# Optimization experiments

Hardware: AMD Instinct MI355X
Metric: run time of the kernel (lower is better)

## Reference

```python
import jax, jax.numpy as jnp
import numpy as np

B, CIN, COUT, RES, WDIM, K, GN_GROUPS = 8, 512, 512, 64, 512, 3, 32


def setup_inputs() -> dict:
    key = jax.random.key(0)
    ks = jax.random.split(key, 6)
    return dict(
        x=jax.random.normal(ks[0], (B, CIN, RES, RES), jnp.float32),
        w=jax.random.normal(ks[1], (B, WDIM), jnp.float32),
        noise=jax.random.normal(ks[2], (B, 1, RES, RES), jnp.float32),
        weight=jax.random.normal(ks[3], (COUT, CIN, K, K), jnp.float32),
        bias=jnp.zeros((COUT,), jnp.float32),
        affine_W=jax.random.normal(ks[4], (3 * CIN, WDIM), jnp.float32),
        affine_b=jnp.ones((3 * CIN,), jnp.float32),  # bias_init=1
        gn_weight=jnp.ones((CIN,), jnp.float32),
        gn_bias=jnp.zeros((CIN,), jnp.float32),
        gamma=jnp.full((1, COUT, 1, 1), 1e-5, jnp.float32),  # layer_scale_init
        noise_strength=jnp.asarray(0.1, jnp.float32),
    )


def _group_norm_f32(x, weight, bias, groups=GN_GROUPS, eps=1e-5):
    # GroupNorm_float32: normalize in float32, cast back to x.dtype
    b, c, h, w = x.shape
    xf = x.astype(jnp.float32).reshape(b, groups, c // groups, h, w)
    mu = xf.mean(axis=(2, 3, 4), keepdims=True)
    var = xf.var(axis=(2, 3, 4), keepdims=True)
    xn = ((xf - mu) * jax.lax.rsqrt(var + eps)).reshape(b, c, h, w)
    return (xn * weight[None, :, None, None] + bias[None, :, None, None]).astype(x.dtype)


def reference(x, w, noise, weight, bias, affine_W, affine_b, gn_weight, gn_bias, gamma, noise_strength):
    b, cin, h, wd = x.shape
    cout, _, kh, kw = weight.shape
    # StyleSplit: FullyConnectedLayer (weight scaled by 1/sqrt(in_features)) then m1*m2+m3
    s = w @ (affine_W.T / jnp.sqrt(jnp.float32(w.shape[1]))) + affine_b  # [B, 3*Cin]
    m1, m2, m3 = jnp.split(s, 3, axis=1)
    styles = m1 * m2 + m3  # [B, Cin]
    # residual path: GroupNorm (float32) first
    xn = _group_norm_f32(x, gn_weight, gn_bias)
    # modulated_conv2d (fused path): per-sample modulate + demodulate
    wmod = weight[None] * styles[:, None, :, None, None]                 # [B,Cout,Cin,K,K]
    dcoef = jax.lax.rsqrt(jnp.sum(jnp.square(wmod), axis=(2, 3, 4)) + 1e-8)  # [B,Cout]
    wmod = wmod * dcoef[:, :, None, None, None]
    # grouped conv with groups = batch (StyleGAN batch-as-groups trick)
    xg = xn.reshape(1, b * cin, h, wd)
    wg = wmod.reshape(b * cout, cin, kh, kw)
    pad = kh // 2
    y = jax.lax.conv_general_dilated(
        xg, wg, window_strides=(1, 1), padding=[(pad, pad), (pad, pad)],
        dimension_numbers=('NCHW', 'OIHW', 'NCHW'), feature_group_count=b)
    y = y.reshape(b, cout, h, wd)
    # noise injection
    y = y + noise * noise_strength
    # fused bias + lrelu with gain = bias_def_gain['lrelu'] * gain = sqrt(2) * 2
    act_gain = np.sqrt(2.0) * 2.0
    y = jax.nn.leaky_relu(y + bias[None, :, None, None], 0.2) * act_gain
    # layer-scale + residual (residual uses the normalized x) * sqrt(2)
    y = (gamma * y + xn) * np.sqrt(2.0)
    return y
```

## Files before the change

kernel.cpp:

```cpp
#include <hip/hip_runtime.h>
#include <hip/hip_bf16.h>

typedef short short8 __attribute__((ext_vector_type(8)));
typedef float f32x4 __attribute__((ext_vector_type(4)));

#define SWZ(c) (((c) & 3) ^ (((c) >> 2) & 3))

static __device__ __forceinline__ unsigned short f2bf(float f) {
    union { float f; unsigned u; } v; v.f = f;
    unsigned r = v.u + 0x7FFFu + ((v.u >> 16) & 1u);
    return (unsigned short)(r >> 16);
}

static __device__ __forceinline__ void gload16(const void* g, void* l) {
    __builtin_amdgcn_global_load_lds(
        (const __attribute__((address_space(1))) unsigned int*)g,
        (__attribute__((address_space(3))) unsigned int*)l, 16, 0, 0);
}

__global__ __launch_bounds__(256) void stylesk(
    const float* __restrict__ w, const float* __restrict__ affW,
    const float* __restrict__ affb, float* __restrict__ styles)
{
    int bx = blockIdx.x, b = blockIdx.y;
    int lane = threadIdx.x & 63, wv = threadIdx.x >> 6;
    float wr[8];
    const float* wb = w + b * 512 + lane * 8;
#pragma unroll
    for (int r = 0; r < 8; ++r) wr[r] = wb[r];
    for (int ii = 0; ii < 4; ++ii) {
        int i = bx * 16 + wv * 4 + ii;
        float d[3];
#pragma unroll
        for (int jj = 0; jj < 3; ++jj) {
            const float* a = affW + (size_t)(jj * 512 + i) * 512 + lane * 8;
            float dd = 0.f;
#pragma unroll
            for (int r = 0; r < 8; ++r) dd += wr[r] * a[r];
            for (int off = 32; off; off >>= 1) dd += __shfl_xor(dd, off);
            d[jj] = dd;
        }
        if (lane == 0) {
            const float inv = 0.044194173824159216f;
            float s0 = d[0] * inv + affb[i];
            float s1 = d[1] * inv + affb[512 + i];
            float s2 = d[2] * inv + affb[1024 + i];
            styles[b * 512 + i] = s0 * s1 + s2;
        }
    }
}

__global__ __launch_bounds__(256) void gnstats(
    const float* __restrict__ x, float* __restrict__ meanv, float* __restrict__ rstdv)
{
    int bx = blockIdx.x, t = threadIdx.x;
    const float4* p = (const float4*)(x + (size_t)bx * 65536);
    float s = 0.f, q = 0.f;
#pragma unroll 4
    for (int k = 0; k < 64; ++k) {
        float4 v = p[t + (k << 8)];
        s += v.x + v.y + v.z + v.w;
        q += v.x * v.x + v.y * v.y + v.z * v.z + v.w * v.w;
    }
    for (int off = 32; off; off >>= 1) { s += __shfl_xor(s, off); q += __shfl_xor(q, off); }
    __shared__ float rs[4], rq[4];
    if ((t & 63) == 0) { rs[t >> 6] = s; rq[t >> 6] = q; }
    __syncthreads();
    if (t == 0) {
        float S = rs[0] + rs[1] + rs[2] + rs[3];
        float Q = rq[0] + rq[1] + rq[2] + rq[3];
        float mu = S * (1.f / 65536.f);
        float var = Q * (1.f / 65536.f) - mu * mu;
        meanv[bx] = mu;
        rstdv[bx] = rsqrtf(var + 1e-5f);
    }
}

__global__ __launch_bounds__(256) void dcoefk(
    const float* __restrict__ weight, const float* __restrict__ styles,
    float* __restrict__ dcoef)
{
    __shared__ float st2[8 * 512];
    __shared__ float red[32];
    int co = blockIdx.x, t = threadIdx.x;
    for (int i = t; i < 4096; i += 256) { float s = styles[i]; st2[i] = s * s; }
    __syncthreads();
    float p[8] = {0, 0, 0, 0, 0, 0, 0, 0};
#pragma unroll
    for (int half = 0; half < 2; ++half) {
        int ci = t * 2 + half;
        const float* wp = weight + ((size_t)co * 512 + ci) * 9;
        float wsq = 0.f;
#pragma unroll
        for (int k = 0; k < 9; ++k) wsq += wp[k] * wp[k];
#pragma unroll
        for (int b = 0; b < 8; ++b) p[b] += wsq * st2[b * 512 + ci];
    }
    int lane = t & 63, wv = t >> 6;
#pragma unroll
    for (int b = 0; b < 8; ++b) {
        float v = p[b];
        for (int off = 32; off; off >>= 1) v += __shfl_xor(v, off);
        if (lane == 0) red[wv * 8 + b] = v;
    }
    __syncthreads();
    if (t < 8) {
        float s = red[t] + red[8 + t] + red[16 + t] + red[24 + t];
        dcoef[t * 512 + co] = rsqrtf(s + 1e-8f);
    }
}

__global__ __launch_bounds__(256) void packk(
    const float* __restrict__ weight, unsigned short* __restrict__ wpk)
{
    __shared__ float ld[9 * 128];
    int co = blockIdx.x, c4 = blockIdx.y, t = threadIdx.x;
    const float* src = weight + (size_t)co * 4608 + c4 * 1152;
    for (int f = t; f < 1152; f += 256)
        ld[(f % 9) * 128 + (f / 9)] = src[f];
    __syncthreads();
    unsigned short* dst = wpk + (size_t)co * 4608 + c4 * 128;
    for (int f = t; f < 1152; f += 256) {
        int tap = f >> 7, ci = f & 127;
        dst[tap * 512 + ci] = f2bf(ld[tap * 128 + ci]);
    }
}

__global__ __launch_bounds__(256) void modpack(
    const float* __restrict__ x, const float* __restrict__ styles,
    const float* __restrict__ gnw, const float* __restrict__ gnb,
    const float* __restrict__ meanv, const float* __restrict__ rstdv,
    unsigned short* __restrict__ xm)
{
    __shared__ float sA[512], sB[512];
    __shared__ unsigned short tr[32 * 520];
    int t = threadIdx.x;
    int px0 = blockIdx.x * 32, b = blockIdx.y;
    for (int i = t; i < 512; i += 256) {
        int g = i >> 4;
        float mu = meanv[b * 32 + g], r = rstdv[b * 32 + g];
        float st = styles[b * 512 + i];
        float a = r * gnw[i];
        sA[i] = a * st;
        sB[i] = (gnb[i] - mu * a) * st;
    }
    __syncthreads();
    int p = t & 31, cb = t >> 5;
    const float* xb = x + (size_t)b * 512 * 4096 + px0 + p;
#pragma unroll 4
    for (int it = 0; it < 64; ++it) {
        int ci = cb + (it << 3);
        float v = xb[(size_t)ci * 4096];
        tr[p * 520 + ci] = f2bf(v * sA[ci] + sB[ci]);
    }
    __syncthreads();
    int gran = t & 63;
#pragma unroll
    for (int k = 0; k < 8; ++k) {
        int pl = k * 4 + (t >> 6);
        short8 v = *(const short8*)&tr[pl * 520 + gran * 8];
        *(short8*)&xm[((size_t)(b * 4096 + px0 + pl) << 9) + gran * 8] = v;
    }
}

__global__ __launch_bounds__(512, 2) void conv3(
    const unsigned short* __restrict__ xm, const unsigned short* __restrict__ wpk,
    const unsigned short* __restrict__ zp,
    const float* __restrict__ x, const float* __restrict__ noise,
    const float* __restrict__ bias, const float* __restrict__ gnw,
    const float* __restrict__ gnb, const float* __restrict__ gamma,
    const float* __restrict__ dcoef, const float* __restrict__ meanv,
    const float* __restrict__ rstdv, const float* __restrict__ nsp,
    float* __restrict__ out)
{
    extern __shared__ char smem[];
    char* wlds = smem;
    char* ilds = smem + 49152;

    const int tid = threadIdx.x, lane = tid & 63, wv = tid >> 6;
    const int ct = blockIdx.x, pt = blockIdx.y, b = blockIdx.z;
    const int co0 = ct * 128, h0 = pt * 8;
    const int wm = wv >> 2, wn = wv & 3;
    const int lm = lane & 15, lg = lane >> 4;

    if (tid < 160) {
        int sel = tid / 80, rem = tid % 80;
        int r = rem >> 3, col = ((rem >> 2) & 1) * 65, g = rem & 3;
        *(short8*)(ilds + sel * 42240 + r * 4224 + col * 64 + g * 16) = (short8)0;
    }

    const unsigned short* wsrc_fix[3]; int wdst_off[3];
#pragma unroll
    for (int q = 0; q < 3; ++q) {
        int k = q * 8 + wv;
        int id = k * 64 + lane;
        int dxid = id >> 9, co = (id >> 2) & 127, g = (id & 3) ^ SWZ(co);
        wsrc_fix[q] = wpk + (size_t)(co0 + co) * 4608 + dxid * 512 + g * 8;
        wdst_off[q] = k * 1024;
    }
    const unsigned short* isrc_fix[5]; int idst_off[5];
#pragma unroll
    for (int q = 0; q < 5; ++q) {
        int k = q * 8 + wv;
        int r = k >> 2, chunk = k & 3;
        int idx = chunk * 64 + lane;
        int cimg = idx >> 2, gs = (idx & 3) ^ SWZ(cimg + 1);
        int imgrow = h0 - 1 + r;
        isrc_fix[q] = ((unsigned)imgrow < 64u)
            ? xm + (((size_t)(b * 4096 + imgrow * 64 + cimg)) << 9) + gs * 8
            : zp;
        idst_off[q] = r * 4224 + 64 + chunk * 1024;
    }

    int aoff[4];
#pragma unroll
    for (int m = 0; m < 4; ++m) {
        int col = wm * 64 + m * 16 + lm;
        aoff[m] = col * 64 + (lg ^ SWZ(col)) * 16;
    }
    int boff[3][4];
#pragma unroll
    for (int dx = 0; dx < 3; ++dx)
#pragma unroll
        for (int nc = 0; nc < 4; ++nc) {
            int c = nc * 16 + lm + dx;
            boff[dx][nc] = c * 64 + (lg ^ SWZ(c)) * 16;
        }

    f32x4 acc[4][8];
#pragma unroll
    for (int m = 0; m < 4; ++m)
#pragma unroll
        for (int n = 0; n < 8; ++n) acc[m][n] = (f32x4){0.f, 0.f, 0.f, 0.f};

#pragma unroll
    for (int q = 0; q < 3; ++q) gload16(wsrc_fix[q], wlds + wdst_off[q]);
#pragma unroll
    for (int q = 0; q < 5; ++q) gload16(isrc_fix[q], ilds + idst_off[q]);
    __syncthreads();

    int cc = 0, dy = 0;
    for (int p = 0; p < 48; ++p) {
        int dyn = dy + 1, ccn = cc;
        if (dyn == 3) { dyn = 0; ccn = cc + 1; }
        if (p < 47) {
            int wadd = dyn * 1536 + ccn * 32;
            char* wd = wlds + ((p + 1) & 1) * 24576;
#pragma unroll
            for (int q = 0; q < 3; ++q) gload16(wsrc_fix[q] + wadd, wd + wdst_off[q]);
        }
        if (dy == 0 && cc < 15) {
            int iadd = (cc + 1) * 32;
            char* idp = ilds + ((cc + 1) & 1) * 42240;
#pragma unroll
            for (int q = 0; q < 5; ++q) gload16(isrc_fix[q] + iadd, idp + idst_off[q]);
        }
        char* wbase = wlds + (p & 1) * 24576;
        char* ibase = ilds + (cc & 1) * 42240 + (2 * wn + dy) * 4224;
#pragma unroll
        for (int dx = 0; dx < 3; ++dx) {
            short8 af[4], bv[8];
#pragma unroll
            for (int m = 0; m < 4; ++m)
                af[m] = *(const short8*)(wbase + dx * 8192 + aoff[m]);
#pragma unroll
            for (int n = 0; n < 8; ++n)
                bv[n] = *(const short8*)(ibase + (n >> 2) * 4224 + boff[dx][n & 3]);
#pragma unroll
            for (int m = 0; m < 4; ++m)
#pragma unroll
                for (int n = 0; n < 8; ++n)
                    acc[m][n] = __builtin_amdgcn_mfma_f32_16x16x32_bf16(
                        af[m], bv[n], acc[m][n], 0, 0, 0);
        }
        __syncthreads();
        dy = dyn; cc = ccn;
    }

    const float nsv = *nsp;
#pragma unroll
    for (int m = 0; m < 4; ++m) {
#pragma unroll
        for (int n = 0; n < 8; ++n) {
            int pix = (h0 + 2 * wn + (n >> 2)) * 64 + (n & 3) * 16 + lm;
            float nz = noise[b * 4096 + pix] * nsv;
#pragma unroll
            for (int j = 0; j < 4; ++j) {
                int co = co0 + wm * 64 + m * 16 + lg * 4 + j;
                int gidx = co >> 4;
                float v = acc[m][n][j] * dcoef[b * 512 + co] + nz + bias[co];
                float act = (v > 0.f ? v : 0.2f * v) * 2.8284271247461903f;
                float xv = x[((size_t)(b * 512 + co)) * 4096 + pix];
                float xn = (xv - meanv[b * 32 + gidx]) * rstdv[b * 32 + gidx] * gnw[co] + gnb[co];
                out[((size_t)(b * 512 + co)) * 4096 + pix] =
                    (gamma[co] * act + xn) * 1.4142135623730951f;
            }
        }
    }
}

extern "C" void kernel_launch(void* const* d_in, const int* in_sizes, int n_in,
                              void* d_out, int out_size, void* d_ws, size_t ws_size,
                              hipStream_t stream) {
    const float* x      = (const float*)d_in[0];
    const float* w      = (const float*)d_in[1];
    const float* noise  = (const float*)d_in[2];
    const float* weight = (const float*)d_in[3];
    const float* bias   = (const float*)d_in[4];
    const float* affW   = (const float*)d_in[5];
    const float* affb   = (const float*)d_in[6];
    const float* gnw    = (const float*)d_in[7];
    const float* gnb    = (const float*)d_in[8];
    const float* gamma  = (const float*)d_in[9];
    const float* nsp    = (const float*)d_in[10];
    float* out = (float*)d_out;

    char* ws = (char*)d_ws;
    float* styles = (float*)(ws + 0);
    float* dcoef  = (float*)(ws + 16384);
    float* meanv  = (float*)(ws + 32768);
    float* rstdv  = (float*)(ws + 33792);
    unsigned short* zp  = (unsigned short*)(ws + 34816);
    unsigned short* wpk = (unsigned short*)(ws + 38912);
    unsigned short* xm  = (unsigned short*)(ws + 4757504);

    hipMemsetAsync(zp, 0, 4096, stream);

    hipFuncSetAttribute(reinterpret_cast<const void*>(conv3),
                        hipFuncAttributeMaxDynamicSharedMemorySize, 135168);

    stylesk<<<dim3(32, 8), 256, 0, stream>>>(w, affW, affb, styles);
    gnstats<<<dim3(256), 256, 0, stream>>>(x, meanv, rstdv);
    packk<<<dim3(512, 4), 256, 0, stream>>>(weight, wpk);
    dcoefk<<<dim3(512), 256, 0, stream>>>(weight, styles, dcoef);
    modpack<<<dim3(128, 8), 256, 0, stream>>>(x, styles, gnw, gnb, meanv, rstdv, xm);
    conv3<<<dim3(4, 8, 8), 512, 133632, stream>>>(xm, wpk, zp, x, noise, bias, gnw, gnb,
                                                  gamma, dcoef, meanv, rstdv, nsp, out);
}
```

Measured before the change: 309.5 us.

## Merge prep kernels and triple-buffer conv weight staging with manual waitcnt pipeline

The five small preprocessing kernels and the memset become two launches that dispatch on block index: stats, styles, weight pack and zero fill in the first, dcoef and activation modpack in the second. This cuts launch gaps. The conv main loop is unrolled into explicit phases per dy, with a third weight LDS buffer and manual s_waitcnt vmcnt/s_barrier in place of __syncthreads. It also interleaves LDS fragment loads with MFMAs under s_setprio so global prefetch runs further ahead. LDS use rises to about 158KB per block, which may limit occupancy, and the hand-counted vmcnt values risk subtle races.

```diff
diff --git a/kernel.cpp b/kernel.cpp
--- a/kernel.cpp
+++ b/kernel.cpp
@@ -5,6 +5,7 @@
 typedef float f32x4 __attribute__((ext_vector_type(4)));
 
 #define SWZ(c) (((c) & 3) ^ (((c) >> 2) & 3))
+#define UNROLL _Pragma("unroll")
 
 static __device__ __forceinline__ unsigned short f2bf(float f) {
     union { float f; unsigned u; } v; v.f = f;
@@ -18,150 +19,189 @@
         (__attribute__((address_space(3))) unsigned int*)l, 16, 0, 0);
 }
 
-__global__ __launch_bounds__(256) void stylesk(
-    const float* __restrict__ w, const float* __restrict__ affW,
-    const float* __restrict__ affb, float* __restrict__ styles)
+__global__ __launch_bounds__(256) void prep1(
+    const float* __restrict__ x, const float* __restrict__ w,
+    const float* __restrict__ affW, const float* __restrict__ affb,
+    const float* __restrict__ weight,
+    float* __restrict__ styles, float* __restrict__ meanv,
+    float* __restrict__ rstdv, unsigned short* __restrict__ wpk,
+    unsigned short* __restrict__ zp)
 {
-    int bx = blockIdx.x, b = blockIdx.y;
-    int lane = threadIdx.x & 63, wv = threadIdx.x >> 6;
-    float wr[8];
-    const float* wb = w + b * 512 + lane * 8;
-#pragma unroll
-    for (int r = 0; r < 8; ++r) wr[r] = wb[r];
-    for (int ii = 0; ii < 4; ++ii) {
-        int i = bx * 16 + wv * 4 + ii;
-        float d[3];
-#pragma unroll
-        for (int jj = 0; jj < 3; ++jj) {
-            const float* a = affW + (size_t)(jj * 512 + i) * 512 + lane * 8;
-            float dd = 0.f;
-#pragma unroll
-            for (int r = 0; r < 8; ++r) dd += wr[r] * a[r];
-            for (int off = 32; off; off >>= 1) dd += __shfl_xor(dd, off);
-            d[jj] = dd;
-        }
-        if (lane == 0) {
-            const float inv = 0.044194173824159216f;
-            float s0 = d[0] * inv + affb[i];
-            float s1 = d[1] * inv + affb[512 + i];
-            float s2 = d[2] * inv + affb[1024 + i];
-            styles[b * 512 + i] = s0 * s1 + s2;
-        }
-    }
-}
-
-__global__ __launch_bounds__(256) void gnstats(
-    const float* __restrict__ x, float* __restrict__ meanv, float* __restrict__ rstdv)
-{
-    int bx = blockIdx.x, t = threadIdx.x;
-    const float4* p = (const float4*)(x + (size_t)bx * 65536);
-    float s = 0.f, q = 0.f;
+    __shared__ float ld[9 * 128];
+    __shared__ float rs[4], rq[4];
+    const int bid = blockIdx.x, t = threadIdx.x;
+
+    if (bid < 256) {
+        const float4* p = (const float4*)(x + (size_t)bid * 65536);
+        float s = 0.f, q = 0.f;
 #pragma unroll 4
-    for (int k = 0; k < 64; ++k) {
-        float4 v = p[t + (k << 8)];
-        s += v.x + v.y + v.z + v.w;
-        q += v.x * v.x + v.y * v.y + v.z * v.z + v.w * v.w;
-    }
-    for (int off = 32; off; off >>= 1) { s += __shfl_xor(s, off); q += __shfl_xor(q, off); }
-    __shared__ float rs[4], rq[4];
-    if ((t & 63) == 0) { rs[t >> 6] = s; rq[t >> 6] = q; }
-    __syncthreads();
-    if (t == 0) {
-        float S = rs[0] + rs[1] + rs[2] + rs[3];
-        float Q = rq[0] + rq[1] + rq[2] + rq[3];
-        float mu = S * (1.f / 65536.f);
-        float var = Q * (1.f / 65536.f) - mu * mu;
-        meanv[bx] = mu;
-        rstdv[bx] = rsqrtf(var + 1e-5f);
-    }
-}
-
-__global__ __launch_bounds__(256) void dcoefk(
-    const float* __restrict__ weight, const float* __restrict__ styles,
-    float* __restrict__ dcoef)
+        for (int k = 0; k < 64; ++k) {
+            float4 v = p[t + (k << 8)];
+            s += v.x + v.y + v.z + v.w;
+            q += v.x * v.x + v.y * v.y + v.z * v.z + v.w * v.w;
+        }
+        for (int off = 32; off; off >>= 1) { s += __shfl_xor(s, off); q += __shfl_xor(q, off); }
+        if ((t & 63) == 0) { rs[t >> 6] = s; rq[t >> 6] = q; }
+        __syncthreads();
+        if (t == 0) {
+            float S = rs[0] + rs[1] + rs[2] + rs[3];
+            float Q = rq[0] + rq[1] + rq[2] + rq[3];
+            float mu = S * (1.f / 65536.f);
+            float var = Q * (1.f / 65536.f) - mu * mu;
+            meanv[bid] = mu;
+            rstdv[bid] = rsqrtf(var + 1e-5f);
+        }
+    } else if (bid < 512) {
+        int idx = bid - 256, bx = idx & 31, b = idx >> 5;
+        int lane = t & 63, wv = t >> 6;
+        float wr[8];
+        const float* wb = w + b * 512 + lane * 8;
+        UNROLL for (int r = 0; r < 8; ++r) wr[r] = wb[r];
+        for (int ii = 0; ii < 4; ++ii) {
+            int i = bx * 16 + wv * 4 + ii;
+            float d[3];
+            UNROLL for (int jj = 0; jj < 3; ++jj) {
+                const float* a = affW + (size_t)(jj * 512 + i) * 512 + lane * 8;
+                float dd = 0.f;
+                UNROLL for (int r = 0; r < 8; ++r) dd += wr[r] * a[r];
+                for (int off = 32; off; off >>= 1) dd += __shfl_xor(dd, off);
+                d[jj] = dd;
+            }
+            if (lane == 0) {
+                const float inv = 0.044194173824159216f;
+                float s0 = d[0] * inv + affb[i];
+                float s1 = d[1] * inv + affb[512 + i];
+                float s2 = d[2] * inv + affb[1024 + i];
+                styles[b * 512 + i] = s0 * s1 + s2;
+            }
+        }
+    } else if (bid < 2560) {
+        int idx = bid - 512, co = idx >> 2, c4 = idx & 3;
+        const float* src = weight + (size_t)co * 4608 + c4 * 1152;
+        for (int f = t; f < 1152; f += 256)
+            ld[(f % 9) * 128 + (f / 9)] = src[f];
+        __syncthreads();
+        unsigned short* dst = wpk + (size_t)co * 4608 + c4 * 128;
+        for (int f = t; f < 1152; f += 256) {
+            int tap = f >> 7, ci = f & 127;
+            dst[tap * 512 + ci] = f2bf(ld[tap * 128 + ci]);
+        }
+    } else {
+        *(short8*)&zp[t * 8] = (short8)0;
+    }
+}
+
+__global__ __launch_bounds__(256) void prep2(
+    const float* __restrict__ x, const float* __restrict__ weight,
+    const float* __restrict__ styles, const float* __restrict__ gnw,
+    const float* __restrict__ gnb, const float* __restrict__ meanv,
+    const float* __restrict__ rstdv,
+    float* __restrict__ dcoef, unsigned short* __restrict__ xm)
 {
     __shared__ float st2[8 * 512];
     __shared__ float red[32];
-    int co = blockIdx.x, t = threadIdx.x;
-    for (int i = t; i < 4096; i += 256) { float s = styles[i]; st2[i] = s * s; }
-    __syncthreads();
-    float p[8] = {0, 0, 0, 0, 0, 0, 0, 0};
-#pragma unroll
-    for (int half = 0; half < 2; ++half) {
-        int ci = t * 2 + half;
-        const float* wp = weight + ((size_t)co * 512 + ci) * 9;
-        float wsq = 0.f;
-#pragma unroll
-        for (int k = 0; k < 9; ++k) wsq += wp[k] * wp[k];
-#pragma unroll
-        for (int b = 0; b < 8; ++b) p[b] += wsq * st2[b * 512 + ci];
-    }
-    int lane = t & 63, wv = t >> 6;
-#pragma unroll
-    for (int b = 0; b < 8; ++b) {
-        float v = p[b];
-        for (int off = 32; off; off >>= 1) v += __shfl_xor(v, off);
-        if (lane == 0) red[wv * 8 + b] = v;
-    }
-    __syncthreads();
-    if (t < 8) {
-        float s = red[t] + red[8 + t] + red[16 + t] + red[24 + t];
-        dcoef[t * 512 + co] = rsqrtf(s + 1e-8f);
-    }
-}
-
-__global__ __launch_bounds__(256) void packk(
-    const float* __restrict__ weight, unsigned short* __restrict__ wpk)
-{
-    __shared__ float ld[9 * 128];
-    int co = blockIdx.x, c4 = blockIdx.y, t = threadIdx.x;
-    const float* src = weight + (size_t)co * 4608 + c4 * 1152;
-    for (int f = t; f < 1152; f += 256)
-        ld[(f % 9) * 128 + (f / 9)] = src[f];
-    __syncthreads();
-    unsigned short* dst = wpk + (size_t)co * 4608 + c4 * 128;
-    for (int f = t; f < 1152; f += 256) {
-        int tap = f >> 7, ci = f & 127;
-        dst[tap * 512 + ci] = f2bf(ld[tap * 128 + ci]);
-    }
-}
-
-__global__ __launch_bounds__(256) void modpack(
-    const float* __restrict__ x, const float* __restrict__ styles,
-    const float* __restrict__ gnw, const float* __restrict__ gnb,
-    const float* __restrict__ meanv, const float* __restrict__ rstdv,
-    unsigned short* __restrict__ xm)
-{
     __shared__ float sA[512], sB[512];
     __shared__ unsigned short tr[32 * 520];
-    int t = threadIdx.x;
-    int px0 = blockIdx.x * 32, b = blockIdx.y;
-    for (int i = t; i < 512; i += 256) {
-        int g = i >> 4;
-        float mu = meanv[b * 32 + g], r = rstdv[b * 32 + g];
-        float st = styles[b * 512 + i];
-        float a = r * gnw[i];
-        sA[i] = a * st;
-        sB[i] = (gnb[i] - mu * a) * st;
-    }
-    __syncthreads();
-    int p = t & 31, cb = t >> 5;
-    const float* xb = x + (size_t)b * 512 * 4096 + px0 + p;
+    const int bid = blockIdx.x, t = threadIdx.x;
+
+    if (bid < 512) {
+        int co = bid;
+        for (int i = t; i < 4096; i += 256) { float s = styles[i]; st2[i] = s * s; }
+        __syncthreads();
+        float p[8] = {0, 0, 0, 0, 0, 0, 0, 0};
+        UNROLL for (int half = 0; half < 2; ++half) {
+            int ci = t * 2 + half;
+            const float* wp = weight + ((size_t)co * 512 + ci) * 9;
+            float wsq = 0.f;
+            UNROLL for (int k = 0; k < 9; ++k) wsq += wp[k] * wp[k];
+            UNROLL for (int b = 0; b < 8; ++b) p[b] += wsq * st2[b * 512 + ci];
+        }
+        int lane = t & 63, wv = t >> 6;
+        UNROLL for (int b = 0; b < 8; ++b) {
+            float v = p[b];
+            for (int off = 32; off; off >>= 1) v += __shfl_xor(v, off);
+            if (lane == 0) red[wv * 8 + b] = v;
+        }
+        __syncthreads();
+        if (t < 8) {
+            float s = red[t] + red[8 + t] + red[16 + t] + red[24 + t];
+            dcoef[t * 512 + co] = rsqrtf(s + 1e-8f);
+        }
+    } else {
+        int idx = bid - 512, b = idx >> 7, px0 = (idx & 127) * 32;
+        for (int i = t; i < 512; i += 256) {
+            int g = i >> 4;
+            float mu = meanv[b * 32 + g], r = rstdv[b * 32 + g];
+            float st = styles[b * 512 + i];
+            float a = r * gnw[i];
+            sA[i] = a * st;
+            sB[i] = (gnb[i] - mu * a) * st;
+        }
+        __syncthreads();
+        int p = t & 31, cb = t >> 5;
+        const float* xb = x + (size_t)b * 512 * 4096 + px0 + p;
 #pragma unroll 4
-    for (int it = 0; it < 64; ++it) {
-        int ci = cb + (it << 3);
-        float v = xb[(size_t)ci * 4096];
-        tr[p * 520 + ci] = f2bf(v * sA[ci] + sB[ci]);
-    }
-    __syncthreads();
-    int gran = t & 63;
-#pragma unroll
-    for (int k = 0; k < 8; ++k) {
-        int pl = k * 4 + (t >> 6);
-        short8 v = *(const short8*)&tr[pl * 520 + gran * 8];
-        *(short8*)&xm[((size_t)(b * 4096 + px0 + pl) << 9) + gran * 8] = v;
-    }
-}
+        for (int it = 0; it < 64; ++it) {
+            int ci = cb + (it << 3);
+            float v = xb[(size_t)ci * 4096];
+            tr[p * 520 + ci] = f2bf(v * sA[ci] + sB[ci]);
+        }
+        __syncthreads();
+        int gran = t & 63;
+        UNROLL for (int k = 0; k < 8; ++k) {
+            int pl = k * 4 + (t >> 6);
+            short8 v = *(const short8*)&tr[pl * 520 + gran * 8];
+            *(short8*)&xm[((size_t)(b * 4096 + px0 + pl) << 9) + gran * 8] = v;
+        }
+    }
+}
+
+#define STAGE_W(SLOT, CC_, DY_)                                                 \
+    { char* wd_ = wlds + (SLOT) * 24576; int wadd_ = (DY_) * 1536 + (CC_) * 32; \
+      UNROLL for (int q = 0; q < 3; ++q)                                        \
+          gload16(wsrc_fix[q] + wadd_, wd_ + wdst_off[q]); }
+
+#define STAGE_I(CC_)                                                            \
+    { char* id_ = ilds + ((CC_) & 1) * 42240; int iadd_ = (CC_) * 32;           \
+      UNROLL for (int q = 0; q < 5; ++q)                                        \
+          gload16(isrc_fix[q] + iadd_, id_ + idst_off[q]); }
+
+#define PHASE(DY, CCSEL, VMN, STAGES_)                                          \
+  {                                                                             \
+    char* wbase = wlds + (DY) * 24576;                                          \
+    char* ibase = ilds + (CCSEL) * 42240 + (2 * wn + (DY)) * 4224;              \
+    short8 a0[4], b0[8], a1[4], b1[8], a2[4], b2[8];                            \
+    UNROLL for (int m = 0; m < 4; ++m)                                          \
+        a0[m] = *(const short8*)(wbase + aoff[m]);                              \
+    UNROLL for (int n = 0; n < 8; ++n)                                          \
+        b0[n] = *(const short8*)(ibase + (n >> 2) * 4224 + boff[0][n & 3]);     \
+    STAGES_                                                                     \
+    asm volatile("s_barrier" ::: "memory");                                     \
+    UNROLL for (int m = 0; m < 4; ++m)                                          \
+        a1[m] = *(const short8*)(wbase + 8192 + aoff[m]);                       \
+    UNROLL for (int n = 0; n < 8; ++n)                                          \
+        b1[n] = *(const short8*)(ibase + (n >> 2) * 4224 + boff[1][n & 3]);     \
+    __builtin_amdgcn_s_setprio(1);                                              \
+    UNROLL for (int m = 0; m < 4; ++m)                                          \
+        UNROLL for (int n = 0; n < 8; ++n)                                      \
+            acc[m][n] = __builtin_amdgcn_mfma_f32_16x16x32_bf16(                \
+                a0[m], b0[n], acc[m][n], 0, 0, 0);                              \
+    UNROLL for (int m = 0; m < 4; ++m)                                          \
+        a2[m] = *(const short8*)(wbase + 16384 + aoff[m]);                      \
+    UNROLL for (int n = 0; n < 8; ++n)                                          \
+        b2[n] = *(const short8*)(ibase + (n >> 2) * 4224 + boff[2][n & 3]);     \
+    UNROLL for (int m = 0; m < 4; ++m)                                          \
+        UNROLL for (int n = 0; n < 8; ++n)                                      \
+            acc[m][n] = __builtin_amdgcn_mfma_f32_16x16x32_bf16(                \
+                a1[m], b1[n], acc[m][n], 0, 0, 0);                              \
+    UNROLL for (int m = 0; m < 4; ++m)                                          \
+        UNROLL for (int n = 0; n < 8; ++n)                                      \
+            acc[m][n] = __builtin_amdgcn_mfma_f32_16x16x32_bf16(                \
+                a2[m], b2[n], acc[m][n], 0, 0, 0);                              \
+    __builtin_amdgcn_s_setprio(0);                                              \
+    asm volatile("s_waitcnt vmcnt(" #VMN ")" ::: "memory");                     \
+    asm volatile("s_barrier" ::: "memory");                                     \
+  }
 
 __global__ __launch_bounds__(512, 2) void conv3(
     const unsigned short* __restrict__ xm, const unsigned short* __restrict__ wpk,
@@ -175,7 +215,7 @@
 {
     extern __shared__ char smem[];
     char* wlds = smem;
-    char* ilds = smem + 49152;
+    char* ilds = smem + 73728;
 
     const int tid = threadIdx.x, lane = tid & 63, wv = tid >> 6;
     const int ct = blockIdx.x, pt = blockIdx.y, b = blockIdx.z;
@@ -190,8 +230,7 @@
     }
 
     const unsigned short* wsrc_fix[3]; int wdst_off[3];
-#pragma unroll
-    for (int q = 0; q < 3; ++q) {
+    UNROLL for (int q = 0; q < 3; ++q) {
         int k = q * 8 + wv;
         int id = k * 64 + lane;
         int dxid = id >> 9, co = (id >> 2) & 127, g = (id & 3) ^ SWZ(co);
@@ -199,8 +238,7 @@
         wdst_off[q] = k * 1024;
     }
     const unsigned short* isrc_fix[5]; int idst_off[5];
-#pragma unroll
-    for (int q = 0; q < 5; ++q) {
+    UNROLL for (int q = 0; q < 5; ++q) {
         int k = q * 8 + wv;
         int r = k >> 2, chunk = k & 3;
         int idx = chunk * 64 + lane;
@@ -213,79 +251,45 @@
     }
 
     int aoff[4];
-#pragma unroll
-    for (int m = 0; m < 4; ++m) {
+    UNROLL for (int m = 0; m < 4; ++m) {
         int col = wm * 64 + m * 16 + lm;
         aoff[m] = col * 64 + (lg ^ SWZ(col)) * 16;
     }
     int boff[3][4];
-#pragma unroll
-    for (int dx = 0; dx < 3; ++dx)
-#pragma unroll
-        for (int nc = 0; nc < 4; ++nc) {
+    UNROLL for (int dx = 0; dx < 3; ++dx)
+        UNROLL for (int nc = 0; nc < 4; ++nc) {
             int c = nc * 16 + lm + dx;
             boff[dx][nc] = c * 64 + (lg ^ SWZ(c)) * 16;
         }
 
     f32x4 acc[4][8];
-#pragma unroll
-    for (int m = 0; m < 4; ++m)
-#pragma unroll
-        for (int n = 0; n < 8; ++n) acc[m][n] = (f32x4){0.f, 0.f, 0.f, 0.f};
-
-#pragma unroll
-    for (int q = 0; q < 3; ++q) gload16(wsrc_fix[q], wlds + wdst_off[q]);
-#pragma unroll
-    for (int q = 0; q < 5; ++q) gload16(isrc_fix[q], ilds + idst_off[q]);
-    __syncthreads();
-
-    int cc = 0, dy = 0;
-    for (int p = 0; p < 48; ++p) {
-        int dyn = dy + 1, ccn = cc;
-        if (dyn == 3) { dyn = 0; ccn = cc + 1; }
-        if (p < 47) {
-            int wadd = dyn * 1536 + ccn * 32;
-            char* wd = wlds + ((p + 1) & 1) * 24576;
-#pragma unroll
-            for (int q = 0; q < 3; ++q) gload16(wsrc_fix[q] + wadd, wd + wdst_off[q]);
-        }
-        if (dy == 0 && cc < 15) {
-            int iadd = (cc + 1) * 32;
-            char* idp = ilds + ((cc + 1) & 1) * 42240;
-#pragma unroll
-            for (int q = 0; q < 5; ++q) gload16(isrc_fix[q] + iadd, idp + idst_off[q]);
-        }
-        char* wbase = wlds + (p & 1) * 24576;
-        char* ibase = ilds + (cc & 1) * 42240 + (2 * wn + dy) * 4224;
-#pragma unroll
-        for (int dx = 0; dx < 3; ++dx) {
-            short8 af[4], bv[8];
-#pragma unroll
-            for (int m = 0; m < 4; ++m)
-                af[m] = *(const short8*)(wbase + dx * 8192 + aoff[m]);
-#pragma unroll
-            for (int n = 0; n < 8; ++n)
-                bv[n] = *(const short8*)(ibase + (n >> 2) * 4224 + boff[dx][n & 3]);
-#pragma unroll
-            for (int m = 0; m < 4; ++m)
-#pragma unroll
-                for (int n = 0; n < 8; ++n)
-                    acc[m][n] = __builtin_amdgcn_mfma_f32_16x16x32_bf16(
-                        af[m], bv[n], acc[m][n], 0, 0, 0);
-        }
-        __syncthreads();
-        dy = dyn; cc = ccn;
-    }
+    UNROLL for (int m = 0; m < 4; ++m)
+        UNROLL for (int n = 0; n < 8; ++n) acc[m][n] = (f32x4){0.f, 0.f, 0.f, 0.f};
+
+    STAGE_W(0, 0, 0)
+    STAGE_I(0)
+    STAGE_W(1, 0, 1)
+    asm volatile("s_waitcnt lgkmcnt(0)" ::: "memory");
+    asm volatile("s_waitcnt vmcnt(3)" ::: "memory");
+    asm volatile("s_barrier" ::: "memory");
+
+#pragma unroll 1
+    for (int cc = 0; cc < 15; ++cc) {
+        const int cs = cc & 1;
+        PHASE(0, cs, 8, STAGE_W(2, cc, 2) STAGE_I(cc + 1))
+        PHASE(1, cs, 8, STAGE_W(0, cc + 1, 0))
+        PHASE(2, cs, 3, STAGE_W(1, cc + 1, 1))
+    }
+    PHASE(0, 1, 3, STAGE_W(2, 15, 2))
+    PHASE(1, 1, 0, {})
+    PHASE(2, 1, 0, {})
 
     const float nsv = *nsp;
-#pragma unroll
-    for (int m = 0; m < 4; ++m) {
-#pragma unroll
-        for (int n = 0; n < 8; ++n) {
+    UNROLL for (int m = 0; m < 4; ++m) {
+        UNROLL for (int n = 0; n < 8; ++n) {
             int pix = (h0 + 2 * wn + (n >> 2)) * 64 + (n & 3) * 16 + lm;
             float nz = noise[b * 4096 + pix] * nsv;
-#pragma unroll
-            for (int j = 0; j < 4; ++j) {
+            UNROLL for (int j = 0; j < 4; ++j) {
                 int co = co0 + wm * 64 + m * 16 + lg * 4 + j;
                 int gidx = co >> 4;
                 float v = acc[m][n][j] * dcoef[b * 512 + co] + nz + bias[co];
@@ -324,16 +328,13 @@
     unsigned short* wpk = (unsigned short*)(ws + 38912);
     unsigned short* xm  = (unsigned short*)(ws + 4757504);
 
-    hipMemsetAsync(zp, 0, 4096, stream);
-
     hipFuncSetAttribute(reinterpret_cast<const void*>(conv3),
-                        hipFuncAttributeMaxDynamicSharedMemorySize, 135168);
-
-    stylesk<<<dim3(32, 8), 256, 0, stream>>>(w, affW, affb, styles);
-    gnstats<<<dim3(256), 256, 0, stream>>>(x, meanv, rstdv);
-    packk<<<dim3(512, 4), 256, 0, stream>>>(weight, wpk);
-    dcoefk<<<dim3(512), 256, 0, stream>>>(weight, styles, dcoef);
-    modpack<<<dim3(128, 8), 256, 0, stream>>>(x, styles, gnw, gnb, meanv, rstdv, xm);
-    conv3<<<dim3(4, 8, 8), 512, 133632, stream>>>(xm, wpk, zp, x, noise, bias, gnw, gnb,
+                        hipFuncAttributeMaxDynamicSharedMemorySize, 158208);
+
+    prep1<<<dim3(2561), 256, 0, stream>>>(x, w, affW, affb, weight,
+                                          styles, meanv, rstdv, wpk, zp);
+    prep2<<<dim3(1536), 256, 0, stream>>>(x, weight, styles, gnw, gnb,
+                                          meanv, rstdv, dcoef, xm);
+    conv3<<<dim3(4, 8, 8), 512, 158208, stream>>>(xm, wpk, zp, x, noise, bias, gnw, gnb,
                                                   gamma, dcoef, meanv, rstdv, nsp, out);
 }
```

Result: faster. 302.4 us (-2.3%).
